# Optimization experiments

Hardware: AMD Instinct MI355X
Metric: run time of the kernel (lower is better)

## Reference

```python
import jax, jax.numpy as jnp
import numpy as np

EMB = 1024
HID = 1024

def setup_inputs() -> dict:
    key = jax.random.key(0)
    ks = jax.random.split(key, 7)
    x = jax.random.normal(ks[0], (4, 2048, EMB), dtype=jnp.float32)
    s = 1.0 / np.sqrt(EMB)
    Wq = jax.random.normal(ks[1], (EMB, HID), dtype=jnp.float32) * s
    bq = jnp.zeros((HID,), dtype=jnp.float32)
    Wk = jax.random.normal(ks[2], (EMB, HID), dtype=jnp.float32) * s
    bk = jnp.zeros((HID,), dtype=jnp.float32)
    Wv = jax.random.normal(ks[3], (EMB, HID), dtype=jnp.float32) * s
    bv = jnp.zeros((HID,), dtype=jnp.float32)
    return {"x": x, "Wq": Wq, "bq": bq, "Wk": Wk, "bk": bk, "Wv": Wv, "bv": bv}

def reference(x, Wq, bq, Wk, bk, Wv, bv):
    # x: [B, S, E]
    B, S, _ = x.shape
    Q = x @ Wq + bq  # [B, S, H]
    K = x @ Wk + bk
    V = x @ Wv + bv
    scale = 1.0 / jnp.sqrt(jnp.asarray(Wq.shape[1], dtype=x.dtype))
    scores = jnp.einsum('bqh,bkh->bqk', Q, K) * scale  # [B, S, S]
    causal = jnp.tril(jnp.ones((S, S), dtype=bool))
    scores = jnp.where(causal, scores, -jnp.inf)
    weights = jax.nn.softmax(scores, axis=-1)
    return jnp.einsum('bqk,bkh->bqh', weights, V)
```

## Files before the change

kernel.cpp:

```cpp
#include <hip/hip_runtime.h>
#include <hip/hip_bf16.h>

typedef __attribute__((ext_vector_type(8))) short bf16x8;
typedef __attribute__((ext_vector_type(4))) float f32x4;
typedef __attribute__((ext_vector_type(4))) unsigned short us4;

#define B_ 4
#define S_ 2048
#define E_ 1024
#define H_ 1024
#define M_ (B_ * S_)
#define N3_ (3 * H_)
#define NTILE_ 16
#define NTRI_ 136

__device__ __forceinline__ unsigned short f2bf(float f) {
  union { float f; unsigned u; } v; v.f = f;
  unsigned r = v.u + 0x7fffu + ((v.u >> 16) & 1u);
  return (unsigned short)(r >> 16);
}
__device__ __forceinline__ float bf2f(unsigned short u) {
  union { unsigned u; float f; } v; v.u = ((unsigned)u) << 16; return v.f;
}

__global__ __launch_bounds__(256) void k_convert_x(const float* __restrict__ x,
                                                   unsigned short* __restrict__ xb) {
  int i = blockIdx.x * 256 + threadIdx.x;
  const float4 v = reinterpret_cast<const float4*>(x)[i];
  us4 o;
  o[0] = f2bf(v.x); o[1] = f2bf(v.y); o[2] = f2bf(v.z); o[3] = f2bf(v.w);
  reinterpret_cast<us4*>(xb)[i] = o;
}

__global__ __launch_bounds__(256) void k_transpose_w(const float* __restrict__ Wq,
                                                     const float* __restrict__ Wk,
                                                     const float* __restrict__ Wv,
                                                     unsigned short* __restrict__ Wt) {
  __shared__ float tile[32][33];
  const int mat = blockIdx.z;
  const float* W = (mat == 0) ? Wq : (mat == 1) ? Wk : Wv;
  const int n0 = blockIdx.x * 32, k0 = blockIdx.y * 32;
  const int tx = threadIdx.x, ty = threadIdx.y;
#pragma unroll
  for (int i = 0; i < 32; i += 8)
    tile[ty + i][tx] = W[(size_t)(k0 + ty + i) * H_ + n0 + tx];
  __syncthreads();
#pragma unroll
  for (int i = 0; i < 32; i += 8) {
    int n = n0 + ty + i;
    Wt[(size_t)(mat * H_ + n) * E_ + k0 + tx] = f2bf(tile[tx][ty + i]);
  }
}

__global__ __launch_bounds__(256, 2) void k_gemm_qkv(
    const unsigned short* __restrict__ xb, const unsigned short* __restrict__ Wt,
    const float* __restrict__ bq, const float* __restrict__ bk,
    const float* __restrict__ bv,
    unsigned short* __restrict__ Qb, unsigned short* __restrict__ Kb,
    unsigned short* __restrict__ Vt) {
  __shared__ unsigned short As[128 * 64];
  __shared__ unsigned short Bs[128 * 64];
  const int nwg = gridDim.x;
  const int cpx = nwg >> 3;
  int bid = blockIdx.x;
  bid = (bid & 7) * cpx + (bid >> 3);
  const int tm = bid / 24, tn = bid % 24;
  const int gm = tm * 128, gn = tn * 128;
  const int tid = threadIdx.x, w = tid >> 6, lane = tid & 63;
  const int wr = w >> 1, wc = w & 1;
  const int srow = lane >> 3;
  const int schunk = (lane & 7) ^ srow;

  f32x4 acc[4][4];
#pragma unroll
  for (int i = 0; i < 4; ++i)
#pragma unroll
    for (int j = 0; j < 4; ++j) acc[i][j] = (f32x4)0.0f;

  for (int kt = 0; kt < 16; ++kt) {
    const int k0 = kt * 64;
#pragma unroll
    for (int i = 0; i < 4; ++i) {
      const int row = w * 32 + i * 8 + srow;
      __builtin_amdgcn_global_load_lds(
          (const __attribute__((address_space(1))) unsigned int*)(xb + (size_t)(gm + row) * E_ + k0 + schunk * 8),
          (__attribute__((address_space(3))) unsigned int*)(As + (w * 32 + i * 8) * 64),
          16, 0, 0);
    }
#pragma unroll
    for (int i = 0; i < 4; ++i) {
      const int row = w * 32 + i * 8 + srow;
      __builtin_amdgcn_global_load_lds(
          (const __attribute__((address_space(1))) unsigned int*)(Wt + (size_t)(gn + row) * E_ + k0 + schunk * 8),
          (__attribute__((address_space(3))) unsigned int*)(Bs + (w * 32 + i * 8) * 64),
          16, 0, 0);
    }
    __syncthreads();
#pragma unroll
    for (int ks = 0; ks < 2; ++ks) {
      bf16x8 af[4], bfrag[4];
#pragma unroll
      for (int mt = 0; mt < 4; ++mt) {
        const int r16 = wr * 64 + mt * 16 + (lane & 15);
        const int ch = (ks * 4 + (lane >> 4)) ^ (r16 & 7);
        af[mt] = *reinterpret_cast<const bf16x8*>(&As[r16 * 64 + ch * 8]);
      }
#pragma unroll
      for (int nt = 0; nt < 4; ++nt) {
        const int c16 = wc * 64 + nt * 16 + (lane & 15);
        const int ch = (ks * 4 + (lane >> 4)) ^ (c16 & 7);
        bfrag[nt] = *reinterpret_cast<const bf16x8*>(&Bs[c16 * 64 + ch * 8]);
      }
#pragma unroll
      for (int mt = 0; mt < 4; ++mt)
#pragma unroll
        for (int nt = 0; nt < 4; ++nt)
          acc[mt][nt] = __builtin_amdgcn_mfma_f32_16x16x32_bf16(
              af[mt], bfrag[nt], acc[mt][nt], 0, 0, 0);
    }
    __syncthreads();
  }

  const int matid = gn >> 10;
  const float* bias = (matid == 0) ? bq : (matid == 1) ? bk : bv;
#pragma unroll
  for (int mt = 0; mt < 4; ++mt) {
#pragma unroll
    for (int nt = 0; nt < 4; ++nt) {
      const int row0 = gm + wr * 64 + mt * 16 + (lane >> 4) * 4;
      const int col = gn + wc * 64 + nt * 16 + (lane & 15);
      const int h = col & 1023;
      const float bb = bias[h];
      if (matid < 2) {
        unsigned short* dst = matid ? Kb : Qb;
#pragma unroll
        for (int r = 0; r < 4; ++r)
          dst[(size_t)(row0 + r) * H_ + h] = f2bf(acc[mt][nt][r] + bb);
      } else {
        const int bat = row0 >> 11, s0 = row0 & 2047;
        us4 pk;
#pragma unroll
        for (int r = 0; r < 4; ++r) pk[r] = f2bf(acc[mt][nt][r] + bb);
        *reinterpret_cast<us4*>(&Vt[(size_t)bat * H_ * S_ + (size_t)h * S_ + s0]) = pk;
      }
    }
  }
}

__global__ __launch_bounds__(256, 2) void k_gemm_scores(
    const unsigned short* __restrict__ Qb, const unsigned short* __restrict__ Kb,
    unsigned short* __restrict__ Pt) {
  __shared__ unsigned short As[128 * 64];
  __shared__ unsigned short Bs[128 * 64];
  const int bid = blockIdx.x;
  const int batch = bid >> 8, t = bid & 255;
  const int tm = t >> 4, tn = t & 15;
  if (tn > tm) return;
  const int gm = tm * 128, gn = tn * 128;
  const int tid = threadIdx.x, w = tid >> 6, lane = tid & 63;
  const int wr = w >> 1, wc = w & 1;
  const int srow = lane >> 3;
  const int schunk = (lane & 7) ^ srow;
  const unsigned short* Abase = Qb + (size_t)batch * S_ * H_;
  const unsigned short* Bbase = Kb + (size_t)batch * S_ * H_;

  f32x4 acc[4][4];
#pragma unroll
  for (int i = 0; i < 4; ++i)
#pragma unroll
    for (int j = 0; j < 4; ++j) acc[i][j] = (f32x4)0.0f;

  for (int kt = 0; kt < 16; ++kt) {
    const int k0 = kt * 64;
#pragma unroll
    for (int i = 0; i < 4; ++i) {
      const int row = w * 32 + i * 8 + srow;
      __builtin_amdgcn_global_load_lds(
          (const __attribute__((address_space(1))) unsigned int*)(Abase + (size_t)(gm + row) * H_ + k0 + schunk * 8),
          (__attribute__((address_space(3))) unsigned int*)(As + (w * 32 + i * 8) * 64),
          16, 0, 0);
      __builtin_amdgcn_global_load_lds(
          (const __attribute__((address_space(1))) unsigned int*)(Bbase + (size_t)(gn + row) * H_ + k0 + schunk * 8),
          (__attribute__((address_space(3))) unsigned int*)(Bs + (w * 32 + i * 8) * 64),
          16, 0, 0);
    }
    __syncthreads();
#pragma unroll
    for (int ks = 0; ks < 2; ++ks) {
      bf16x8 af[4], bfrag[4];
#pragma unroll
      for (int mt = 0; mt < 4; ++mt) {
        const int r16 = wr * 64 + mt * 16 + (lane & 15);
        const int ch = (ks * 4 + (lane >> 4)) ^ (r16 & 7);
        af[mt] = *reinterpret_cast<const bf16x8*>(&As[r16 * 64 + ch * 8]);
      }
#pragma unroll
      for (int nt = 0; nt < 4; ++nt) {
        const int c16 = wc * 64 + nt * 16 + (lane & 15);
        const int ch = (ks * 4 + (lane >> 4)) ^ (c16 & 7);
        bfrag[nt] = *reinterpret_cast<const bf16x8*>(&Bs[c16 * 64 + ch * 8]);
      }
#pragma unroll
      for (int mt = 0; mt < 4; ++mt)
#pragma unroll
        for (int nt = 0; nt < 4; ++nt)
          acc[mt][nt] = __builtin_amdgcn_mfma_f32_16x16x32_bf16(
              af[mt], bfrag[nt], acc[mt][nt], 0, 0, 0);
    }
    __syncthreads();
  }

  const size_t tbase = ((size_t)batch * NTRI_ + (tm * (tm + 1)) / 2 + tn) * 16384;
#pragma unroll
  for (int mt = 0; mt < 4; ++mt) {
#pragma unroll
    for (int nt = 0; nt < 4; ++nt) {
      const int row0 = wr * 64 + mt * 16 + (lane >> 4) * 4;
      const int col = wc * 64 + nt * 16 + (lane & 15);
#pragma unroll
      for (int r = 0; r < 4; ++r)
        Pt[tbase + (size_t)(row0 + r) * 128 + col] = f2bf(acc[mt][nt][r] * 0.03125f);
    }
  }
}

__global__ __launch_bounds__(256) void k_softmax(unsigned short* __restrict__ Pt) {
  const int tid = threadIdx.x, lane = tid & 63;
  const int gr = blockIdx.x * 4 + (tid >> 6);
  const int batch = gr >> 11, q = gr & 2047;
  const int tm = q >> 7, r = q & 127;
  const int W = (tm + 1) << 7;
  const size_t rowb = ((size_t)batch * NTRI_ + (tm * (tm + 1)) / 2) * 16384 + (size_t)r * 128;

  float s[32];
  float mx = -1e30f;
#pragma unroll
  for (int it = 0; it < 4; ++it) {
    const int c = it * 512 + lane * 8;
    if (c < W) {
      const int tn = c >> 7;
      const bf16x8 v = *reinterpret_cast<const bf16x8*>(&Pt[rowb + (size_t)tn * 16384 + (c & 127)]);
#pragma unroll
      for (int j = 0; j < 8; ++j) {
        float f = bf2f((unsigned short)v[j]);
        if (c + j > q) f = -1e30f;
        s[it * 8 + j] = f;
        mx = fmaxf(mx, f);
      }
    } else {
#pragma unroll
      for (int j = 0; j < 8; ++j) s[it * 8 + j] = -1e30f;
    }
  }
#pragma unroll
  for (int off = 32; off; off >>= 1) mx = fmaxf(mx, __shfl_xor(mx, off));
  float sum = 0.f;
#pragma unroll
  for (int it = 0; it < 4; ++it)
#pragma unroll
    for (int j = 0; j < 8; ++j) {
      const float p = __expf(s[it * 8 + j] - mx);
      s[it * 8 + j] = p;
      sum += p;
    }
#pragma unroll
  for (int off = 32; off; off >>= 1) sum += __shfl_xor(sum, off);
  const float inv = 1.0f / sum;
#pragma unroll
  for (int it = 0; it < 4; ++it) {
    const int c = it * 512 + lane * 8;
    if (c < W) {
      const int tn = c >> 7;
      bf16x8 o;
#pragma unroll
      for (int j = 0; j < 8; ++j) o[j] = (short)f2bf(s[it * 8 + j] * inv);
      *reinterpret_cast<bf16x8*>(&Pt[rowb + (size_t)tn * 16384 + (c & 127)]) = o;
    }
  }
}

__global__ __launch_bounds__(256, 2) void k_gemm_pv(
    const unsigned short* __restrict__ Pt, const unsigned short* __restrict__ Vt,
    float* __restrict__ out) {
  __shared__ unsigned short As[128 * 64];
  __shared__ unsigned short Bs[128 * 64];
  const int bid = blockIdx.x;
  const int batch = bid >> 7, t = bid & 127;
  const int tm = t >> 3, tn = t & 7;
  const int gm = tm * 128, gn = tn * 128;
  const int tid = threadIdx.x, w = tid >> 6, lane = tid & 63;
  const int wr = w >> 1, wc = w & 1;
  const int srow = lane >> 3;
  const int schunk = (lane & 7) ^ srow;
  const size_t trow = ((size_t)batch * NTRI_ + (tm * (tm + 1)) / 2) * 16384;
  const unsigned short* Bbase = Vt + (size_t)batch * H_ * S_;
  const int nk = (tm + 1) * 2;

  f32x4 acc[4][4];
#pragma unroll
  for (int i = 0; i < 4; ++i)
#pragma unroll
    for (int j = 0; j < 4; ++j) acc[i][j] = (f32x4)0.0f;

  for (int kt = 0; kt < nk; ++kt) {
    const int ktn = kt >> 1, cin = (kt & 1) * 64;
#pragma unroll
    for (int i = 0; i < 4; ++i) {
      const int row = w * 32 + i * 8 + srow;
      __builtin_amdgcn_global_load_lds(
          (const __attribute__((address_space(1))) unsigned int*)(Pt + trow + (size_t)ktn * 16384 + (size_t)row * 128 + cin + schunk * 8),
          (__attribute__((address_space(3))) unsigned int*)(As + (w * 32 + i * 8) * 64),
          16, 0, 0);
      __builtin_amdgcn_global_load_lds(
          (const __attribute__((address_space(1))) unsigned int*)(Bbase + (size_t)(gn + row) * S_ + kt * 64 + schunk * 8),
          (__attribute__((address_space(3))) unsigned int*)(Bs + (w * 32 + i * 8) * 64),
          16, 0, 0);
    }
    __syncthreads();
#pragma unroll
    for (int ks = 0; ks < 2; ++ks) {
      bf16x8 af[4], bfrag[4];
#pragma unroll
      for (int mt = 0; mt < 4; ++mt) {
        const int r16 = wr * 64 + mt * 16 + (lane & 15);
        const int ch = (ks * 4 + (lane >> 4)) ^ (r16 & 7);
        af[mt] = *reinterpret_cast<const bf16x8*>(&As[r16 * 64 + ch * 8]);
      }
#pragma unroll
      for (int nt = 0; nt < 4; ++nt) {
        const int c16 = wc * 64 + nt * 16 + (lane & 15);
        const int ch = (ks * 4 + (lane >> 4)) ^ (c16 & 7);
        bfrag[nt] = *reinterpret_cast<const bf16x8*>(&Bs[c16 * 64 + ch * 8]);
      }
#pragma unroll
      for (int mt = 0; mt < 4; ++mt)
#pragma unroll
        for (int nt = 0; nt < 4; ++nt)
          acc[mt][nt] = __builtin_amdgcn_mfma_f32_16x16x32_bf16(
              af[mt], bfrag[nt], acc[mt][nt], 0, 0, 0);
    }
    __syncthreads();
  }

#pragma unroll
  for (int mt = 0; mt < 4; ++mt) {
#pragma unroll
    for (int nt = 0; nt < 4; ++nt) {
      const int row0 = gm + wr * 64 + mt * 16 + (lane >> 4) * 4;
      const int col = gn + wc * 64 + nt * 16 + (lane & 15);
#pragma unroll
      for (int r = 0; r < 4; ++r)
        out[(size_t)batch * S_ * H_ + (size_t)(row0 + r) * H_ + col] = acc[mt][nt][r];
    }
  }
}

extern "C" void kernel_launch(void* const* d_in, const int* in_sizes, int n_in,
                              void* d_out, int out_size, void* d_ws, size_t ws_size,
                              hipStream_t stream) {
  const float* x  = (const float*)d_in[0];
  const float* Wq = (const float*)d_in[1];
  const float* bq = (const float*)d_in[2];
  const float* Wk = (const float*)d_in[3];
  const float* bk = (const float*)d_in[4];
  const float* Wv = (const float*)d_in[5];
  const float* bv = (const float*)d_in[6];
  float* out = (float*)d_out;

  unsigned short* Qb = (unsigned short*)d_ws;
  unsigned short* Kb = Qb + (size_t)M_ * H_;
  unsigned short* Vt = Kb + (size_t)M_ * H_;
  unsigned short* Xr = Vt + (size_t)M_ * H_;
  unsigned short* xb = Xr;
  unsigned short* Wt = Xr + (size_t)M_ * E_;
  unsigned short* Pt = Xr;

  hipLaunchKernelGGL(k_convert_x, dim3(M_ * E_ / 1024), dim3(256), 0, stream, x, xb);
  hipLaunchKernelGGL(k_transpose_w, dim3(32, 32, 3), dim3(32, 8), 0, stream, Wq, Wk, Wv, Wt);
  hipLaunchKernelGGL(k_gemm_qkv, dim3(1536), dim3(256), 0, stream,
                     xb, Wt, bq, bk, bv, Qb, Kb, Vt);
  hipLaunchKernelGGL(k_gemm_scores, dim3(1024), dim3(256), 0, stream, Qb, Kb, Pt);
  hipLaunchKernelGGL(k_softmax, dim3(2048), dim3(256), 0, stream, Pt);
  hipLaunchKernelGGL(k_gemm_pv, dim3(512), dim3(256), 0, stream, Pt, Vt, out);
}
```

Before: 160.0 us.

## Rewrite QKV GEMM as 256x256 8-wave pipelined kernel and reorder attention GEMM grids

The QKV projection GEMM now uses 256x256 tiles with 8 waves, double-buffered LDS and a four-phase schedule. Each phase interleaves half-tile global-to-LDS loads with MFMA work, using explicit barriers, waitcnt and setprio. The scores GEMM launches only lower-triangular tiles with an XCD-aware block remap instead of early-exiting blocks. The PV GEMM orders blocks heaviest-first in a snake pattern to balance the causal workload. The larger tiles need more LDS and registers per block, which can limit occupancy.

```diff
diff --git a/kernel.cpp b/kernel.cpp
--- a/kernel.cpp
+++ b/kernel.cpp
@@ -11,7 +11,6 @@
 #define H_ 1024
 #define M_ (B_ * S_)
 #define N3_ (3 * H_)
-#define NTILE_ 16
 #define NTRI_ 136
 
 __device__ __forceinline__ unsigned short f2bf(float f) {
@@ -52,95 +51,145 @@
   }
 }
 
-__global__ __launch_bounds__(256, 2) void k_gemm_qkv(
+__device__ __forceinline__ void stage_half_A(
+    const unsigned short* gA , int ld,
+    unsigned short* ldsA , int mh, int w, int srow, int schunk) {
+#pragma unroll
+  for (int l = 0; l < 2; ++l) {
+    const int row0 = l * 128 + mh * 64 + w * 8;
+    __builtin_amdgcn_global_load_lds(
+        (const __attribute__((address_space(1))) unsigned int*)(gA + (size_t)(row0 + srow) * ld + schunk * 8),
+        (__attribute__((address_space(3))) unsigned int*)(ldsA + row0 * 64),
+        16, 0, 0);
+  }
+}
+__device__ __forceinline__ void stage_half_B(
+    const unsigned short* gB, int ld,
+    unsigned short* ldsB, int nh, int w, int srow, int schunk) {
+#pragma unroll
+  for (int l = 0; l < 2; ++l) {
+    const int fi = (w * 2 + l) * 8;
+    const int row0 = (fi >> 5) * 64 + nh * 32 + (fi & 31);
+    __builtin_amdgcn_global_load_lds(
+        (const __attribute__((address_space(1))) unsigned int*)(gB + (size_t)(row0 + srow) * ld + schunk * 8),
+        (__attribute__((address_space(3))) unsigned int*)(ldsB + row0 * 64),
+        16, 0, 0);
+  }
+}
+
+#define PHASE(MH, NH, STAGE_STMT, TAIL_STMT)                                     \
+  {                                                                              \
+    bf16x8 af[4][2], bfv[2][2];                                                  \
+    _Pragma("unroll") for (int fm = 0; fm < 4; ++fm) {                           \
+      const int ra = wr * 128 + (MH) * 64 + fm * 16 + l15;                       \
+      const unsigned short* ap = &As[abuf + ra * 64];                            \
+      af[fm][0] = *reinterpret_cast<const bf16x8*>(ap + c0 * 8);                 \
+      af[fm][1] = *reinterpret_cast<const bf16x8*>(ap + c1 * 8);                 \
+    }                                                                            \
+    _Pragma("unroll") for (int fn = 0; fn < 2; ++fn) {                           \
+      const int rb = wc * 64 + (NH) * 32 + fn * 16 + l15;                        \
+      const unsigned short* bp = &Bs[abuf + rb * 64];                            \
+      bfv[fn][0] = *reinterpret_cast<const bf16x8*>(bp + c0 * 8);                \
+      bfv[fn][1] = *reinterpret_cast<const bf16x8*>(bp + c1 * 8);                \
+    }                                                                            \
+    STAGE_STMT;                                                                  \
+    __builtin_amdgcn_s_barrier();                                                \
+    asm volatile("s_waitcnt lgkmcnt(0)" ::: "memory");                           \
+    __builtin_amdgcn_sched_barrier(0);                                           \
+    __builtin_amdgcn_s_setprio(1);                                               \
+    _Pragma("unroll") for (int fm = 0; fm < 4; ++fm)                             \
+      _Pragma("unroll") for (int fn = 0; fn < 2; ++fn) {                         \
+        acc[(MH) * 4 + fm][(NH) * 2 + fn] =                                      \
+            __builtin_amdgcn_mfma_f32_16x16x32_bf16(                             \
+                af[fm][0], bfv[fn][0], acc[(MH) * 4 + fm][(NH) * 2 + fn], 0, 0, 0); \
+        acc[(MH) * 4 + fm][(NH) * 2 + fn] =                                      \
+            __builtin_amdgcn_mfma_f32_16x16x32_bf16(                             \
+                af[fm][1], bfv[fn][1], acc[(MH) * 4 + fm][(NH) * 2 + fn], 0, 0, 0); \
+      }                                                                          \
+    __builtin_amdgcn_s_setprio(0);                                               \
+    TAIL_STMT;                                                                   \
+    __builtin_amdgcn_s_barrier();                                                \
+  }
+
+__global__ __launch_bounds__(512, 2) void k_gemm_qkv8(
     const unsigned short* __restrict__ xb, const unsigned short* __restrict__ Wt,
     const float* __restrict__ bq, const float* __restrict__ bk,
     const float* __restrict__ bv,
     unsigned short* __restrict__ Qb, unsigned short* __restrict__ Kb,
     unsigned short* __restrict__ Vt) {
-  __shared__ unsigned short As[128 * 64];
-  __shared__ unsigned short Bs[128 * 64];
-  const int nwg = gridDim.x;
-  const int cpx = nwg >> 3;
+  __shared__ __align__(16) unsigned short As[2 * 256 * 64];
+  __shared__ __align__(16) unsigned short Bs[2 * 256 * 64];
   int bid = blockIdx.x;
-  bid = (bid & 7) * cpx + (bid >> 3);
-  const int tm = bid / 24, tn = bid % 24;
-  const int gm = tm * 128, gn = tn * 128;
+  bid = (bid & 7) * 48 + (bid >> 3);
+  const int tm = bid / 12, tn = bid % 12;
+  const int gm = tm * 256, gn = tn * 256;
   const int tid = threadIdx.x, w = tid >> 6, lane = tid & 63;
-  const int wr = w >> 1, wc = w & 1;
-  const int srow = lane >> 3;
-  const int schunk = (lane & 7) ^ srow;
-
-  f32x4 acc[4][4];
-#pragma unroll
-  for (int i = 0; i < 4; ++i)
+  const int wr = w >> 2, wc = w & 3;
+  const int l15 = lane & 15, hi = lane >> 4;
+  const int srow = lane >> 3, schunk = (lane & 7) ^ srow;
+  const int c0 = hi ^ (lane & 7), c1 = c0 ^ 4;
+  const unsigned short* gA = xb + (size_t)gm * E_;
+  const unsigned short* gB = Wt + (size_t)gn * E_;
+
+  f32x4 acc[8][4];
+#pragma unroll
+  for (int i = 0; i < 8; ++i)
 #pragma unroll
     for (int j = 0; j < 4; ++j) acc[i][j] = (f32x4)0.0f;
 
-  for (int kt = 0; kt < 16; ++kt) {
-    const int k0 = kt * 64;
-#pragma unroll
-    for (int i = 0; i < 4; ++i) {
-      const int row = w * 32 + i * 8 + srow;
-      __builtin_amdgcn_global_load_lds(
-          (const __attribute__((address_space(1))) unsigned int*)(xb + (size_t)(gm + row) * E_ + k0 + schunk * 8),
-          (__attribute__((address_space(3))) unsigned int*)(As + (w * 32 + i * 8) * 64),
-          16, 0, 0);
-    }
-#pragma unroll
-    for (int i = 0; i < 4; ++i) {
-      const int row = w * 32 + i * 8 + srow;
-      __builtin_amdgcn_global_load_lds(
-          (const __attribute__((address_space(1))) unsigned int*)(Wt + (size_t)(gn + row) * E_ + k0 + schunk * 8),
-          (__attribute__((address_space(3))) unsigned int*)(Bs + (w * 32 + i * 8) * 64),
-          16, 0, 0);
-    }
-    __syncthreads();
-#pragma unroll
-    for (int ks = 0; ks < 2; ++ks) {
-      bf16x8 af[4], bfrag[4];
-#pragma unroll
-      for (int mt = 0; mt < 4; ++mt) {
-        const int r16 = wr * 64 + mt * 16 + (lane & 15);
-        const int ch = (ks * 4 + (lane >> 4)) ^ (r16 & 7);
-        af[mt] = *reinterpret_cast<const bf16x8*>(&As[r16 * 64 + ch * 8]);
-      }
-#pragma unroll
-      for (int nt = 0; nt < 4; ++nt) {
-        const int c16 = wc * 64 + nt * 16 + (lane & 15);
-        const int ch = (ks * 4 + (lane >> 4)) ^ (c16 & 7);
-        bfrag[nt] = *reinterpret_cast<const bf16x8*>(&Bs[c16 * 64 + ch * 8]);
-      }
-#pragma unroll
-      for (int mt = 0; mt < 4; ++mt)
-#pragma unroll
-        for (int nt = 0; nt < 4; ++nt)
-          acc[mt][nt] = __builtin_amdgcn_mfma_f32_16x16x32_bf16(
-              af[mt], bfrag[nt], acc[mt][nt], 0, 0, 0);
-    }
-    __syncthreads();
+  stage_half_A(gA, E_, As, 0, w, srow, schunk);
+  stage_half_A(gA, E_, As, 1, w, srow, schunk);
+  stage_half_B(gB, E_, Bs, 0, w, srow, schunk);
+  stage_half_B(gB, E_, Bs, 1, w, srow, schunk);
+  stage_half_A(gA + 64, E_, As + 16384, 0, w, srow, schunk);
+  stage_half_B(gB + 64, E_, Bs + 16384, 0, w, srow, schunk);
+  asm volatile("s_waitcnt vmcnt(4)" ::: "memory");
+  __builtin_amdgcn_s_barrier();
+
+  for (int k = 0; k < 14; ++k) {
+    const int abuf = (k & 1) << 14;
+    const int nbuf = abuf ^ (1 << 14);
+    PHASE(0, 0, stage_half_A(gA + (k + 1) * 64, E_, As + nbuf, 1, w, srow, schunk), )
+    PHASE(0, 1, stage_half_B(gB + (k + 1) * 64, E_, Bs + nbuf, 1, w, srow, schunk), )
+    PHASE(1, 0, stage_half_A(gA + (k + 2) * 64, E_, As + abuf, 0, w, srow, schunk), )
+    PHASE(1, 1, stage_half_B(gB + (k + 2) * 64, E_, Bs + abuf, 0, w, srow, schunk),
+          asm volatile("s_waitcnt vmcnt(4)" ::: "memory"))
+  }
+  {
+    const int abuf = 0;
+    PHASE(0, 0, stage_half_A(gA + 15 * 64, E_, As + 16384, 1, w, srow, schunk), )
+    PHASE(0, 1, stage_half_B(gB + 15 * 64, E_, Bs + 16384, 1, w, srow, schunk), )
+    PHASE(1, 0, , )
+    PHASE(1, 1, , asm volatile("s_waitcnt vmcnt(0)" ::: "memory"))
+  }
+  {
+    const int abuf = 1 << 14;
+    PHASE(0, 0, , )
+    PHASE(0, 1, , )
+    PHASE(1, 0, , )
+    PHASE(1, 1, , )
   }
 
   const int matid = gn >> 10;
   const float* bias = (matid == 0) ? bq : (matid == 1) ? bk : bv;
 #pragma unroll
-  for (int mt = 0; mt < 4; ++mt) {
-#pragma unroll
-    for (int nt = 0; nt < 4; ++nt) {
-      const int row0 = gm + wr * 64 + mt * 16 + (lane >> 4) * 4;
-      const int col = gn + wc * 64 + nt * 16 + (lane & 15);
+  for (int mf = 0; mf < 8; ++mf) {
+#pragma unroll
+    for (int nf = 0; nf < 4; ++nf) {
+      const int row0 = gm + wr * 128 + mf * 16 + hi * 4;
+      const int col = gn + wc * 64 + nf * 16 + l15;
       const int h = col & 1023;
       const float bb = bias[h];
       if (matid < 2) {
         unsigned short* dst = matid ? Kb : Qb;
 #pragma unroll
         for (int r = 0; r < 4; ++r)
-          dst[(size_t)(row0 + r) * H_ + h] = f2bf(acc[mt][nt][r] + bb);
+          dst[(size_t)(row0 + r) * H_ + h] = f2bf(acc[mf][nf][r] + bb);
       } else {
         const int bat = row0 >> 11, s0 = row0 & 2047;
         us4 pk;
 #pragma unroll
-        for (int r = 0; r < 4; ++r) pk[r] = f2bf(acc[mt][nt][r] + bb);
+        for (int r = 0; r < 4; ++r) pk[r] = f2bf(acc[mf][nf][r] + bb);
         *reinterpret_cast<us4*>(&Vt[(size_t)bat * H_ * S_ + (size_t)h * S_ + s0]) = pk;
       }
     }
@@ -152,10 +201,13 @@
     unsigned short* __restrict__ Pt) {
   __shared__ unsigned short As[128 * 64];
   __shared__ unsigned short Bs[128 * 64];
-  const int bid = blockIdx.x;
-  const int batch = bid >> 8, t = bid & 255;
-  const int tm = t >> 4, tn = t & 15;
-  if (tn > tm) return;
+  int bid = blockIdx.x;
+  bid = (bid & 7) * 68 + (bid >> 3);
+  const int batch = bid / NTRI_;
+  const int t = bid % NTRI_;
+  int tm = 0;
+  while ((tm + 1) * (tm + 2) / 2 <= t) ++tm;
+  const int tn = t - tm * (tm + 1) / 2;
   const int gm = tm * 128, gn = tn * 128;
   const int tid = threadIdx.x, w = tid >> 6, lane = tid & 63;
   const int wr = w >> 1, wc = w & 1;
@@ -284,9 +336,11 @@
     float* __restrict__ out) {
   __shared__ unsigned short As[128 * 64];
   __shared__ unsigned short Bs[128 * 64];
-  const int bid = blockIdx.x;
-  const int batch = bid >> 7, t = bid & 127;
-  const int tm = t >> 3, tn = t & 7;
+  const int b0 = blockIdx.x;
+  const int rk = (b0 < 256) ? b0 : 767 - b0;
+  const int tm = 15 - (rk >> 5);
+  const int batch = (rk >> 3) & 3;
+  const int tn = rk & 7;
   const int gm = tm * 128, gn = tn * 128;
   const int tid = threadIdx.x, w = tid >> 6, lane = tid & 63;
   const int wr = w >> 1, wc = w & 1;
@@ -377,9 +431,9 @@
 
   hipLaunchKernelGGL(k_convert_x, dim3(M_ * E_ / 1024), dim3(256), 0, stream, x, xb);
   hipLaunchKernelGGL(k_transpose_w, dim3(32, 32, 3), dim3(32, 8), 0, stream, Wq, Wk, Wv, Wt);
-  hipLaunchKernelGGL(k_gemm_qkv, dim3(1536), dim3(256), 0, stream,
+  hipLaunchKernelGGL(k_gemm_qkv8, dim3(384), dim3(512), 0, stream,
                      xb, Wt, bq, bk, bv, Qb, Kb, Vt);
-  hipLaunchKernelGGL(k_gemm_scores, dim3(1024), dim3(256), 0, stream, Qb, Kb, Pt);
+  hipLaunchKernelGGL(k_gemm_scores, dim3(544), dim3(256), 0, stream, Qb, Kb, Pt);
   hipLaunchKernelGGL(k_softmax, dim3(2048), dim3(256), 0, stream, Pt);
   hipLaunchKernelGGL(k_gemm_pv, dim3(512), dim3(256), 0, stream, Pt, Vt, out);
 }
```

Measured after the change: 171.5 us. 1.07x slower.

## Widen QKV GEMM tiles, compact causal score grid, balance PV tile order

Applied to the files above, without the earlier changes.

The QKV projection GEMM now uses 128x256 output tiles, so each workgroup computes 4x8 MFMA fragments per wave and loads each x tile half as often. The scores GEMM launches only the 136 lower-triangular tiles per batch, with an XCD-aware block remap instead of early-exiting upper tiles. The PV GEMM reorders blocks so the heaviest row tiles (large tm) are scheduled first, paired in a zigzag with lighter ones, to balance work across CUs. The wider tile raises register and LDS pressure and may reduce occupancy.

```diff
diff --git a/kernel.cpp b/kernel.cpp
--- a/kernel.cpp
+++ b/kernel.cpp
@@ -11,7 +11,6 @@
 #define H_ 1024
 #define M_ (B_ * S_)
 #define N3_ (3 * H_)
-#define NTILE_ 16
 #define NTRI_ 136
 
 __device__ __forceinline__ unsigned short f2bf(float f) {
@@ -59,23 +58,24 @@
     unsigned short* __restrict__ Qb, unsigned short* __restrict__ Kb,
     unsigned short* __restrict__ Vt) {
   __shared__ unsigned short As[128 * 64];
-  __shared__ unsigned short Bs[128 * 64];
-  const int nwg = gridDim.x;
-  const int cpx = nwg >> 3;
+  __shared__ unsigned short Bs[256 * 64];
   int bid = blockIdx.x;
-  bid = (bid & 7) * cpx + (bid >> 3);
-  const int tm = bid / 24, tn = bid % 24;
-  const int gm = tm * 128, gn = tn * 128;
+  bid = (bid & 7) * 96 + (bid >> 3);
+  const int tm = bid / 12, tn = bid % 12;
+  const int gm = tm * 128, gn = tn * 256;
   const int tid = threadIdx.x, w = tid >> 6, lane = tid & 63;
   const int wr = w >> 1, wc = w & 1;
+  const int l15 = lane & 15, hi = lane >> 4;
   const int srow = lane >> 3;
   const int schunk = (lane & 7) ^ srow;
-
-  f32x4 acc[4][4];
+  const unsigned short* gA = xb + (size_t)gm * E_;
+  const unsigned short* gB = Wt + (size_t)gn * E_;
+
+  f32x4 acc[4][8];
 #pragma unroll
   for (int i = 0; i < 4; ++i)
 #pragma unroll
-    for (int j = 0; j < 4; ++j) acc[i][j] = (f32x4)0.0f;
+    for (int j = 0; j < 8; ++j) acc[i][j] = (f32x4)0.0f;
 
   for (int kt = 0; kt < 16; ++kt) {
     const int k0 = kt * 64;
@@ -83,38 +83,38 @@
     for (int i = 0; i < 4; ++i) {
       const int row = w * 32 + i * 8 + srow;
       __builtin_amdgcn_global_load_lds(
-          (const __attribute__((address_space(1))) unsigned int*)(xb + (size_t)(gm + row) * E_ + k0 + schunk * 8),
+          (const __attribute__((address_space(1))) unsigned int*)(gA + (size_t)row * E_ + k0 + schunk * 8),
           (__attribute__((address_space(3))) unsigned int*)(As + (w * 32 + i * 8) * 64),
           16, 0, 0);
     }
 #pragma unroll
-    for (int i = 0; i < 4; ++i) {
-      const int row = w * 32 + i * 8 + srow;
-      __builtin_amdgcn_global_load_lds(
-          (const __attribute__((address_space(1))) unsigned int*)(Wt + (size_t)(gn + row) * E_ + k0 + schunk * 8),
-          (__attribute__((address_space(3))) unsigned int*)(Bs + (w * 32 + i * 8) * 64),
+    for (int i = 0; i < 8; ++i) {
+      const int row = w * 64 + i * 8 + srow;
+      __builtin_amdgcn_global_load_lds(
+          (const __attribute__((address_space(1))) unsigned int*)(gB + (size_t)row * E_ + k0 + schunk * 8),
+          (__attribute__((address_space(3))) unsigned int*)(Bs + (w * 64 + i * 8) * 64),
           16, 0, 0);
     }
     __syncthreads();
 #pragma unroll
     for (int ks = 0; ks < 2; ++ks) {
-      bf16x8 af[4], bfrag[4];
+      bf16x8 af[4], bfrag[8];
 #pragma unroll
       for (int mt = 0; mt < 4; ++mt) {
-        const int r16 = wr * 64 + mt * 16 + (lane & 15);
-        const int ch = (ks * 4 + (lane >> 4)) ^ (r16 & 7);
-        af[mt] = *reinterpret_cast<const bf16x8*>(&As[r16 * 64 + ch * 8]);
-      }
-#pragma unroll
-      for (int nt = 0; nt < 4; ++nt) {
-        const int c16 = wc * 64 + nt * 16 + (lane & 15);
-        const int ch = (ks * 4 + (lane >> 4)) ^ (c16 & 7);
-        bfrag[nt] = *reinterpret_cast<const bf16x8*>(&Bs[c16 * 64 + ch * 8]);
+        const int ra = wr * 64 + mt * 16 + l15;
+        const int ch = (ks * 4 + hi) ^ (ra & 7);
+        af[mt] = *reinterpret_cast<const bf16x8*>(&As[ra * 64 + ch * 8]);
+      }
+#pragma unroll
+      for (int nt = 0; nt < 8; ++nt) {
+        const int rb = wc * 128 + nt * 16 + l15;
+        const int ch = (ks * 4 + hi) ^ (rb & 7);
+        bfrag[nt] = *reinterpret_cast<const bf16x8*>(&Bs[rb * 64 + ch * 8]);
       }
 #pragma unroll
       for (int mt = 0; mt < 4; ++mt)
 #pragma unroll
-        for (int nt = 0; nt < 4; ++nt)
+        for (int nt = 0; nt < 8; ++nt)
           acc[mt][nt] = __builtin_amdgcn_mfma_f32_16x16x32_bf16(
               af[mt], bfrag[nt], acc[mt][nt], 0, 0, 0);
     }
@@ -126,9 +126,9 @@
 #pragma unroll
   for (int mt = 0; mt < 4; ++mt) {
 #pragma unroll
-    for (int nt = 0; nt < 4; ++nt) {
-      const int row0 = gm + wr * 64 + mt * 16 + (lane >> 4) * 4;
-      const int col = gn + wc * 64 + nt * 16 + (lane & 15);
+    for (int nt = 0; nt < 8; ++nt) {
+      const int row0 = gm + wr * 64 + mt * 16 + hi * 4;
+      const int col = gn + wc * 128 + nt * 16 + l15;
       const int h = col & 1023;
       const float bb = bias[h];
       if (matid < 2) {
@@ -152,10 +152,13 @@
     unsigned short* __restrict__ Pt) {
   __shared__ unsigned short As[128 * 64];
   __shared__ unsigned short Bs[128 * 64];
-  const int bid = blockIdx.x;
-  const int batch = bid >> 8, t = bid & 255;
-  const int tm = t >> 4, tn = t & 15;
-  if (tn > tm) return;
+  int bid = blockIdx.x;
+  bid = (bid & 7) * 68 + (bid >> 3);
+  const int batch = bid / NTRI_;
+  const int t = bid % NTRI_;
+  int tm = 0;
+  while ((tm + 1) * (tm + 2) / 2 <= t) ++tm;
+  const int tn = t - tm * (tm + 1) / 2;
   const int gm = tm * 128, gn = tn * 128;
   const int tid = threadIdx.x, w = tid >> 6, lane = tid & 63;
   const int wr = w >> 1, wc = w & 1;
@@ -284,9 +287,11 @@
     float* __restrict__ out) {
   __shared__ unsigned short As[128 * 64];
   __shared__ unsigned short Bs[128 * 64];
-  const int bid = blockIdx.x;
-  const int batch = bid >> 7, t = bid & 127;
-  const int tm = t >> 3, tn = t & 7;
+  const int b0 = blockIdx.x;
+  const int rk = (b0 < 256) ? b0 : 767 - b0;
+  const int tm = 15 - (rk >> 5);
+  const int batch = (rk >> 3) & 3;
+  const int tn = rk & 7;
   const int gm = tm * 128, gn = tn * 128;
   const int tid = threadIdx.x, w = tid >> 6, lane = tid & 63;
   const int wr = w >> 1, wc = w & 1;
@@ -377,9 +382,9 @@
 
   hipLaunchKernelGGL(k_convert_x, dim3(M_ * E_ / 1024), dim3(256), 0, stream, x, xb);
   hipLaunchKernelGGL(k_transpose_w, dim3(32, 32, 3), dim3(32, 8), 0, stream, Wq, Wk, Wv, Wt);
-  hipLaunchKernelGGL(k_gemm_qkv, dim3(1536), dim3(256), 0, stream,
+  hipLaunchKernelGGL(k_gemm_qkv, dim3(768), dim3(256), 0, stream,
                      xb, Wt, bq, bk, bv, Qb, Kb, Vt);
-  hipLaunchKernelGGL(k_gemm_scores, dim3(1024), dim3(256), 0, stream, Qb, Kb, Pt);
+  hipLaunchKernelGGL(k_gemm_scores, dim3(544), dim3(256), 0, stream, Qb, Kb, Pt);
   hipLaunchKernelGGL(k_softmax, dim3(2048), dim3(256), 0, stream, Pt);
   hipLaunchKernelGGL(k_gemm_pv, dim3(512), dim3(256), 0, stream, Pt, Vt, out);
 }
```

After: 154.5 us. 3.4% less time.
